# Kernel tuning notes

Hardware: AMD Instinct MI355X
Metric: run time of the kernel (lower is better)

Reference implementation:

```python
import jax, jax.numpy as jnp
import numpy as np

N, T, E, D, U = 32, 2048, 512, 1024, 256


def setup_inputs() -> dict:
    key = jax.random.key(0)
    ks = jax.random.split(key, 6)
    queries = jax.random.normal(ks[0], (N, 1, D), dtype=jnp.float32)
    prev = jax.random.uniform(ks[1], (N, T), dtype=jnp.float32)
    prev = prev / jnp.sum(prev, axis=1, keepdims=True)  # distribution-like initial alignment
    memory = jax.random.normal(ks[2], (N, T, E), dtype=jnp.float32)
    W_q = jax.random.normal(ks[3], (D, U), dtype=jnp.float32) * (1.0 / np.sqrt(D))
    W_k = jax.random.normal(ks[4], (E, U), dtype=jnp.float32) * (1.0 / np.sqrt(E))
    v = jax.random.uniform(ks[5], (U,), dtype=jnp.float32)
    return {"queries": queries, "previous_alignments": prev, "memory": memory,
            "W_q": W_q, "W_k": W_k, "v": v}


def safe_cumprod_exclusive(x):
    # exclusive cumprod via log-space cumsum, clamped like the torch original
    logsum = jnp.cumsum(jnp.log(jnp.clip(x, 1e-20, 1.0)), axis=1)  # [N,T]
    excl = jnp.concatenate([jnp.zeros_like(logsum[:, :1]), logsum], axis=1)[:, :-1]
    return jnp.exp(excl)


def reference(queries, previous_alignments, memory, W_q, W_k, v):
    # Bahdanau additive score (normalize=False path)
    proj_key = jnp.einsum('bte,eu->btu', memory, W_k)          # set_memory
    proj_q = jnp.einsum('bqd,du->bqu', queries, W_q)           # [N,1,U]
    weights = jnp.einsum('btu,u->bt', jnp.tanh(proj_q + proj_key), v)  # [N,T]
    p_choose = jax.nn.sigmoid(weights)
    # monotonic attention recursion in cumsum/cumprod form
    cumprod_1mp = safe_cumprod_exclusive(1.0 - p_choose)
    alignments = p_choose * cumprod_1mp * jnp.cumsum(
        previous_alignments / jnp.clip(cumprod_1mp, 1e-10, 1.0), axis=1)
    contexts = jnp.einsum('bt,bte->be', alignments, memory)    # bmm + squeeze
    return (contexts, alignments)
```

## Files before the change

kernel.cpp:

```cpp
#include <hip/hip_runtime.h>
#include <math.h>

#define N_ 32
#define T_ 2048
#define E_ 512
#define D_ 1024
#define U_ 256
#define PQ_CH 4

typedef __attribute__((ext_vector_type(8))) short bf16x8;
typedef __attribute__((ext_vector_type(16))) float f32x16;

__device__ __forceinline__ short f2bf_rne(float x) {
  unsigned int u = __float_as_uint(x);
  unsigned int r = u + 0x7FFFu + ((u >> 16) & 1u);
  return (short)(r >> 16);
}
__device__ __forceinline__ short f2bf_trunc(float x) {
  return (short)(__float_as_uint(x) >> 16);
}
__device__ __forceinline__ float bf2f(short h) {
  return __uint_as_float(((unsigned int)(unsigned short)h) << 16);
}

__global__ __launch_bounds__(256) void wk_pack_kernel(
    const float* __restrict__ Wk, bf16x8* __restrict__ whiP, bf16x8* __restrict__ wloP) {
  const int fid = blockIdx.x * 256 + threadIdx.x;
  const int lane = fid & 63;
  const int ub = (fid >> 6) & 7;
  const int kc = (fid >> 9) & 3;
  const int c = fid >> 11;
  const int u = ub * 32 + (lane & 31);
  const int e0 = c * 64 + kc * 16 + (lane >> 5) * 8;
  bf16x8 H, L;
#pragma unroll
  for (int j = 0; j < 8; ++j) {
    float x = Wk[(size_t)(e0 + j) * U_ + u];
    short h = f2bf_trunc(x);
    H[j] = h;
    L[j] = f2bf_rne(x - bf2f(h));
  }
  whiP[fid] = H;
  wloP[fid] = L;
}

__global__ __launch_bounds__(256) void projq_partial_kernel(
    const float* __restrict__ queries, const float* __restrict__ W_q,
    float* __restrict__ pq_part) {
  const int b = blockIdx.y, ch = blockIdx.x, tid = threadIdx.x;
  const int d0 = ch * (D_ / PQ_CH);
  const float* q = queries + b * D_ + d0;
  const float* wq = W_q + (size_t)d0 * U_ + tid;
  float acc = 0.f;
#pragma unroll 8
  for (int d = 0; d < D_ / PQ_CH; ++d)
    acc = fmaf(q[d], wq[(size_t)d * U_], acc);
  pq_part[((b * PQ_CH) + ch) * U_ + tid] = acc;
}

__global__ __launch_bounds__(256) void projq_reduce_kernel(
    const float* __restrict__ pq_part, float* __restrict__ proj_q) {
  const int b = blockIdx.x, tid = threadIdx.x;
  float s = 0.f;
#pragma unroll
  for (int c = 0; c < PQ_CH; ++c) s += pq_part[((b * PQ_CH) + c) * U_ + tid];
  proj_q[b * U_ + tid] = s;
}

__global__ __launch_bounds__(256, 2) void score_kernel(
    const float* __restrict__ memory, const bf16x8* __restrict__ whiP,
    const bf16x8* __restrict__ wloP, const float* __restrict__ proj_q,
    const float* __restrict__ v, float* __restrict__ p_choose) {
  __shared__ short sAhi[2][128 * 64];
  __shared__ short sAlo[2][128 * 64];
  __shared__ float smem_w[4][128];

  const int b = blockIdx.y;
  const int t0 = blockIdx.x * 128;
  const int tid = threadIdx.x;
  const int lane = tid & 63;
  const int ty = tid >> 6;
  const int l31 = lane & 31;
  const int half = lane >> 5;

  f32x16 acc[4][2];
#pragma unroll
  for (int mt = 0; mt < 4; ++mt)
#pragma unroll
    for (int nt = 0; nt < 2; ++nt)
#pragma unroll
      for (int r = 0; r < 16; ++r) acc[mt][nt][r] = 0.f;

  const int sr = tid >> 1;
  const int cs = (tid & 1) * 32;
  const float* srow = memory + ((size_t)(b * T_ + t0 + sr)) * E_ + cs;

  float4 xr[8];
  auto load_chunk = [&](int it) {
    const float* src = srow + it * 64;
#pragma unroll
    for (int j = 0; j < 8; ++j) xr[j] = *(const float4*)(src + j * 4);
  };
  auto stage_chunk = [&](int p) {
    char* bh = (char*)&sAhi[p][0] + sr * 128;
    char* bl = (char*)&sAlo[p][0] + sr * 128;
#pragma unroll
    for (int j = 0; j < 4; ++j) {
      float xs[8] = {xr[2 * j].x, xr[2 * j].y, xr[2 * j].z, xr[2 * j].w,
                     xr[2 * j + 1].x, xr[2 * j + 1].y, xr[2 * j + 1].z, xr[2 * j + 1].w};
      bf16x8 H, L;
#pragma unroll
      for (int i = 0; i < 8; ++i) {
        short h = f2bf_trunc(xs[i]);
        H[i] = h;
        L[i] = f2bf_rne(xs[i] - bf2f(h));
      }
      const int slot = (((tid & 1) * 4 + j) ^ (sr & 7)) * 16;
      *(bf16x8*)(bh + slot) = H;
      *(bf16x8*)(bl + slot) = L;
    }
  };

  load_chunk(0);
  stage_chunk(0);
  __syncthreads();

  for (int it = 0; it < 8; ++it) {
    const int p = it & 1;
    if (it < 7) load_chunk(it + 1);
#pragma unroll
    for (int kc = 0; kc < 4; ++kc) {
      bf16x8 bh[2], bl[2];
#pragma unroll
      for (int nt = 0; nt < 2; ++nt) {
        const int fidx = ((it * 4 + kc) * 8 + (ty * 2 + nt)) * 64 + lane;
        bh[nt] = whiP[fidx];
        bl[nt] = wloP[fidx];
      }
      bf16x8 ah[4], al[4];
#pragma unroll
      for (int mt = 0; mt < 4; ++mt) {
        const int m = mt * 32 + l31;
        const int off = m * 128 + (((kc * 2 + half) ^ (m & 7)) * 16);
        ah[mt] = *(const bf16x8*)((const char*)&sAhi[p][0] + off);
        al[mt] = *(const bf16x8*)((const char*)&sAlo[p][0] + off);
      }
#pragma unroll
      for (int mt = 0; mt < 4; ++mt)
#pragma unroll
        for (int nt = 0; nt < 2; ++nt) {
          acc[mt][nt] = __builtin_amdgcn_mfma_f32_32x32x16_bf16(ah[mt], bh[nt], acc[mt][nt], 0, 0, 0);
          acc[mt][nt] = __builtin_amdgcn_mfma_f32_32x32x16_bf16(ah[mt], bl[nt], acc[mt][nt], 0, 0, 0);
          acc[mt][nt] = __builtin_amdgcn_mfma_f32_32x32x16_bf16(al[mt], bh[nt], acc[mt][nt], 0, 0, 0);
        }
    }
    if (it < 7) {
      stage_chunk(p ^ 1);
      __syncthreads();
    }
  }

  const int u0 = ty * 64 + l31;
  const int u1 = ty * 64 + 32 + l31;
  const float pq0 = proj_q[b * U_ + u0], pq1 = proj_q[b * U_ + u1];
  const float v0 = v[u0], v1 = v[u1];

#pragma unroll
  for (int mt = 0; mt < 4; ++mt)
#pragma unroll
    for (int r = 0; r < 16; ++r) {
      float s = tanhf(acc[mt][0][r] + pq0) * v0 + tanhf(acc[mt][1][r] + pq1) * v1;
#pragma unroll
      for (int off = 1; off < 32; off <<= 1) s += __shfl_xor(s, off, 64);
      if (l31 == 0) {
        const int row = mt * 32 + (r & 3) + 8 * (r >> 2) + 4 * half;
        smem_w[ty][row] = s;
      }
    }
  __syncthreads();
  if (tid < 128) {
    const float w = smem_w[0][tid] + smem_w[1][tid] + smem_w[2][tid] + smem_w[3][tid];
    p_choose[b * T_ + t0 + tid] = 1.0f / (1.0f + expf(-w));
  }
}

__device__ __forceinline__ float block_incl_scan(float val, float* sbuf, int tid) {
  float x = val;
  sbuf[tid] = x;
  __syncthreads();
#pragma unroll
  for (int off = 1; off < 256; off <<= 1) {
    float t = (tid >= off) ? sbuf[tid - off] : 0.f;
    __syncthreads();
    x += t;
    sbuf[tid] = x;
    __syncthreads();
  }
  return x;
}

__global__ __launch_bounds__(256) void scan_kernel(
    const float* __restrict__ p_choose, const float* __restrict__ prev,
    float* __restrict__ align_out) {
  __shared__ float sbuf[256];
  const int b = blockIdx.x, tid = threadIdx.x;
  const int base = b * T_ + tid * 8;
  float4 p0 = *(const float4*)(p_choose + base);
  float4 p1 = *(const float4*)(p_choose + base + 4);
  float p[8] = {p0.x, p0.y, p0.z, p0.w, p1.x, p1.y, p1.z, p1.w};
  float s[8];
  float run = 0.f;
#pragma unroll
  for (int k = 0; k < 8; ++k) {
    float x = 1.0f - p[k];
    x = fminf(fmaxf(x, 1e-20f), 1.0f);
    run += logf(x);
    s[k] = run;
  }
  float incl = block_incl_scan(run, sbuf, tid);
  float excl = incl - run;
  float cp[8];
#pragma unroll
  for (int k = 0; k < 8; ++k)
    cp[k] = expf(excl + (k ? s[k - 1] : 0.f));
  float4 r0 = *(const float4*)(prev + base);
  float4 r1 = *(const float4*)(prev + base + 4);
  float pr[8] = {r0.x, r0.y, r0.z, r0.w, r1.x, r1.y, r1.z, r1.w};
  float s2[8];
  float run2 = 0.f;
#pragma unroll
  for (int k = 0; k < 8; ++k) {
    float d = fminf(fmaxf(cp[k], 1e-10f), 1.0f);
    run2 += pr[k] / d;
    s2[k] = run2;
  }
  float incl2 = block_incl_scan(run2, sbuf, tid);
  float excl2 = incl2 - run2;
#pragma unroll
  for (int k = 0; k < 8; ++k)
    p[k] = p[k] * cp[k] * (excl2 + s2[k]);
  *(float4*)(align_out + base) = make_float4(p[0], p[1], p[2], p[3]);
  *(float4*)(align_out + base + 4) = make_float4(p[4], p[5], p[6], p[7]);
}

__global__ __launch_bounds__(256) void ctx_partial_kernel(
    const float* __restrict__ memory, const float* __restrict__ align,
    float* __restrict__ partials) {
  const int b = blockIdx.y, ch = blockIdx.x, tid = threadIdx.x;
  const int tg = tid >> 7;
  const int col = (tid & 127) * 4;
  const int t0 = ch * 256 + tg * 128;
  const float* mrow = memory + ((size_t)(b * T_ + t0)) * E_ + col;
  const float* arow = align + b * T_ + t0;
  float4 a = make_float4(0.f, 0.f, 0.f, 0.f);
#pragma unroll 4
  for (int t = 0; t < 128; ++t) {
    float al = arow[t];
    float4 m = *(const float4*)(mrow + (size_t)t * E_);
    a.x = fmaf(al, m.x, a.x);
    a.y = fmaf(al, m.y, a.y);
    a.z = fmaf(al, m.z, a.z);
    a.w = fmaf(al, m.w, a.w);
  }
  *(float4*)(partials + ((size_t)(b * 16 + ch * 2 + tg)) * E_ + col) = a;
}

__global__ __launch_bounds__(256) void ctx_reduce_kernel(
    const float* __restrict__ partials, float* __restrict__ ctx) {
  const int b = blockIdx.x, tid = threadIdx.x;
#pragma unroll
  for (int e = tid; e < E_; e += 256) {
    float s = 0.f;
#pragma unroll
    for (int c = 0; c < 16; ++c) s += partials[((size_t)(b * 16 + c)) * E_ + e];
    ctx[b * E_ + e] = s;
  }
}

extern "C" void kernel_launch(void* const* d_in, const int* in_sizes, int n_in,
                              void* d_out, int out_size, void* d_ws, size_t ws_size,
                              hipStream_t stream) {
  (void)in_sizes; (void)n_in; (void)out_size; (void)ws_size;
  const float* queries = (const float*)d_in[0];
  const float* prev    = (const float*)d_in[1];
  const float* memory  = (const float*)d_in[2];
  const float* W_q     = (const float*)d_in[3];
  const float* W_k     = (const float*)d_in[4];
  const float* v       = (const float*)d_in[5];

  float* out = (float*)d_out;
  float* ctx_out = out;
  float* align_out = out + N_ * E_;

  float* ws = (float*)d_ws;
  bf16x8* whiP     = (bf16x8*)ws;
  bf16x8* wloP     = (bf16x8*)(ws + 65536);
  float* p_choose  = ws + 131072;
  float* proj_q    = ws + 196608;
  float* pq_part   = ws + 204800;
  float* ctx_parts = ws;

  wk_pack_kernel<<<dim3(64), 256, 0, stream>>>(W_k, whiP, wloP);
  projq_partial_kernel<<<dim3(PQ_CH, N_), 256, 0, stream>>>(queries, W_q, pq_part);
  projq_reduce_kernel<<<dim3(N_), 256, 0, stream>>>(pq_part, proj_q);
  score_kernel<<<dim3(T_ / 128, N_), 256, 0, stream>>>(memory, whiP, wloP, proj_q, v, p_choose);
  scan_kernel<<<dim3(N_), 256, 0, stream>>>(p_choose, prev, align_out);
  ctx_partial_kernel<<<dim3(8, N_), 256, 0, stream>>>(memory, align_out, ctx_parts);
  ctx_reduce_kernel<<<dim3(N_), 256, 0, stream>>>(ctx_parts, ctx_out);
}
```

Measured before the change: 286.3 us.

## Fuse prep kernels, drop score double-buffering, use atomics for context reduction

Merges the W_k packing and the query-projection partial kernels into one launch, and folds the proj_q reduction into the score kernel's epilogue. The score kernel moves from a double-buffered LDS pipeline to a single buffer with two barriers per chunk, which halves its LDS use but no longer overlaps global loads with MFMA work. The context reduction kernel is replaced by float atomicAdds from 512 blocks, with the scan kernel zeroing the output first. This removes three launches, but the atomic sums make results order-dependent and the loss of prefetch may slow the dominant score kernel.

```diff
diff --git a/kernel.cpp b/kernel.cpp
--- a/kernel.cpp
+++ b/kernel.cpp
@@ -6,7 +6,6 @@
 #define E_ 512
 #define D_ 1024
 #define U_ 256
-#define PQ_CH 4
 
 typedef __attribute__((ext_vector_type(8))) short bf16x8;
 typedef __attribute__((ext_vector_type(16))) float f32x16;
@@ -23,56 +22,52 @@
   return __uint_as_float(((unsigned int)(unsigned short)h) << 16);
 }
 
-__global__ __launch_bounds__(256) void wk_pack_kernel(
-    const float* __restrict__ Wk, bf16x8* __restrict__ whiP, bf16x8* __restrict__ wloP) {
-  const int fid = blockIdx.x * 256 + threadIdx.x;
-  const int lane = fid & 63;
-  const int ub = (fid >> 6) & 7;
-  const int kc = (fid >> 9) & 3;
-  const int c = fid >> 11;
-  const int u = ub * 32 + (lane & 31);
-  const int e0 = c * 64 + kc * 16 + (lane >> 5) * 8;
-  bf16x8 H, L;
-#pragma unroll
-  for (int j = 0; j < 8; ++j) {
-    float x = Wk[(size_t)(e0 + j) * U_ + u];
-    short h = f2bf_trunc(x);
-    H[j] = h;
-    L[j] = f2bf_rne(x - bf2f(h));
-  }
-  whiP[fid] = H;
-  wloP[fid] = L;
-}
-
-__global__ __launch_bounds__(256) void projq_partial_kernel(
-    const float* __restrict__ queries, const float* __restrict__ W_q,
-    float* __restrict__ pq_part) {
-  const int b = blockIdx.y, ch = blockIdx.x, tid = threadIdx.x;
-  const int d0 = ch * (D_ / PQ_CH);
-  const float* q = queries + b * D_ + d0;
-  const float* wq = W_q + (size_t)d0 * U_ + tid;
-  float acc = 0.f;
+__global__ __launch_bounds__(256) void prep_kernel(
+    const float* __restrict__ Wk, const float* __restrict__ queries,
+    const float* __restrict__ Wq, bf16x8* __restrict__ whiP,
+    bf16x8* __restrict__ wloP, float* __restrict__ pq_part) {
+  const int wg = blockIdx.x, tid = threadIdx.x;
+  if (wg < 64) {
+    const int fid = wg * 256 + tid;
+    const int lane = fid & 63;
+    const int ub = (fid >> 6) & 7;
+    const int kc = (fid >> 9) & 3;
+    const int c = fid >> 11;
+    const int u = ub * 32 + (lane & 31);
+    const int e0 = c * 64 + kc * 16 + (lane >> 5) * 8;
+    bf16x8 H, L;
+#pragma unroll
+    for (int j = 0; j < 8; ++j) {
+      float x = Wk[(size_t)(e0 + j) * U_ + u];
+      short h = f2bf_trunc(x);
+      H[j] = h;
+      L[j] = f2bf_rne(x - bf2f(h));
+    }
+    whiP[fid] = H;
+    wloP[fid] = L;
+  } else {
+    const int id = wg - 64;
+    const int ch = id & 3;
+    const int b = id >> 2;
+    const int bb = (wg - 64) >> 2;
+    const int d0 = ch * 256;
+    const float* q = queries + bb * D_ + d0;
+    const float* wq = Wq + (size_t)d0 * U_ + tid;
+    float acc = 0.f;
 #pragma unroll 8
-  for (int d = 0; d < D_ / PQ_CH; ++d)
-    acc = fmaf(q[d], wq[(size_t)d * U_], acc);
-  pq_part[((b * PQ_CH) + ch) * U_ + tid] = acc;
-}
-
-__global__ __launch_bounds__(256) void projq_reduce_kernel(
-    const float* __restrict__ pq_part, float* __restrict__ proj_q) {
-  const int b = blockIdx.x, tid = threadIdx.x;
-  float s = 0.f;
-#pragma unroll
-  for (int c = 0; c < PQ_CH; ++c) s += pq_part[((b * PQ_CH) + c) * U_ + tid];
-  proj_q[b * U_ + tid] = s;
+    for (int d = 0; d < 256; ++d)
+      acc = fmaf(q[d], wq[(size_t)d * U_], acc);
+    pq_part[(bb * 4 + ch) * U_ + tid] = acc;
+    (void)b;
+  }
 }
 
 __global__ __launch_bounds__(256, 2) void score_kernel(
     const float* __restrict__ memory, const bf16x8* __restrict__ whiP,
-    const bf16x8* __restrict__ wloP, const float* __restrict__ proj_q,
+    const bf16x8* __restrict__ wloP, const float* __restrict__ pq_part,
     const float* __restrict__ v, float* __restrict__ p_choose) {
-  __shared__ short sAhi[2][128 * 64];
-  __shared__ short sAlo[2][128 * 64];
+  __shared__ short sAhi[128 * 64];
+  __shared__ short sAlo[128 * 64];
   __shared__ float smem_w[4][128];
 
   const int b = blockIdx.y;
@@ -95,39 +90,33 @@
   const int cs = (tid & 1) * 32;
   const float* srow = memory + ((size_t)(b * T_ + t0 + sr)) * E_ + cs;
 
-  float4 xr[8];
-  auto load_chunk = [&](int it) {
+  for (int it = 0; it < 8; ++it) {
+    float4 xr[8];
     const float* src = srow + it * 64;
 #pragma unroll
     for (int j = 0; j < 8; ++j) xr[j] = *(const float4*)(src + j * 4);
-  };
-  auto stage_chunk = [&](int p) {
-    char* bh = (char*)&sAhi[p][0] + sr * 128;
-    char* bl = (char*)&sAlo[p][0] + sr * 128;
-#pragma unroll
-    for (int j = 0; j < 4; ++j) {
-      float xs[8] = {xr[2 * j].x, xr[2 * j].y, xr[2 * j].z, xr[2 * j].w,
-                     xr[2 * j + 1].x, xr[2 * j + 1].y, xr[2 * j + 1].z, xr[2 * j + 1].w};
-      bf16x8 H, L;
-#pragma unroll
-      for (int i = 0; i < 8; ++i) {
-        short h = f2bf_trunc(xs[i]);
-        H[i] = h;
-        L[i] = f2bf_rne(xs[i] - bf2f(h));
-      }
-      const int slot = (((tid & 1) * 4 + j) ^ (sr & 7)) * 16;
-      *(bf16x8*)(bh + slot) = H;
-      *(bf16x8*)(bl + slot) = L;
-    }
-  };
-
-  load_chunk(0);
-  stage_chunk(0);
-  __syncthreads();
-
-  for (int it = 0; it < 8; ++it) {
-    const int p = it & 1;
-    if (it < 7) load_chunk(it + 1);
+    __syncthreads();
+    {
+      char* bhp = (char*)sAhi + sr * 128;
+      char* blp = (char*)sAlo + sr * 128;
+#pragma unroll
+      for (int j = 0; j < 4; ++j) {
+        float xs[8] = {xr[2 * j].x, xr[2 * j].y, xr[2 * j].z, xr[2 * j].w,
+                       xr[2 * j + 1].x, xr[2 * j + 1].y, xr[2 * j + 1].z, xr[2 * j + 1].w};
+        bf16x8 H, L;
+#pragma unroll
+        for (int i = 0; i < 8; ++i) {
+          short h = f2bf_trunc(xs[i]);
+          H[i] = h;
+          L[i] = f2bf_rne(xs[i] - bf2f(h));
+        }
+        const int slot = (((tid & 1) * 4 + j) ^ (sr & 7)) * 16;
+        *(bf16x8*)(bhp + slot) = H;
+        *(bf16x8*)(blp + slot) = L;
+      }
+    }
+    __syncthreads();
+
 #pragma unroll
     for (int kc = 0; kc < 4; ++kc) {
       bf16x8 bh[2], bl[2];
@@ -142,8 +131,8 @@
       for (int mt = 0; mt < 4; ++mt) {
         const int m = mt * 32 + l31;
         const int off = m * 128 + (((kc * 2 + half) ^ (m & 7)) * 16);
-        ah[mt] = *(const bf16x8*)((const char*)&sAhi[p][0] + off);
-        al[mt] = *(const bf16x8*)((const char*)&sAlo[p][0] + off);
+        ah[mt] = *(const bf16x8*)((const char*)sAhi + off);
+        al[mt] = *(const bf16x8*)((const char*)sAlo + off);
       }
 #pragma unroll
       for (int mt = 0; mt < 4; ++mt)
@@ -154,17 +143,17 @@
           acc[mt][nt] = __builtin_amdgcn_mfma_f32_32x32x16_bf16(al[mt], bh[nt], acc[mt][nt], 0, 0, 0);
         }
     }
-    if (it < 7) {
-      stage_chunk(p ^ 1);
-      __syncthreads();
-    }
   }
 
   const int u0 = ty * 64 + l31;
-  const int u1 = ty * 64 + 32 + l31;
-  const float pq0 = proj_q[b * U_ + u0], pq1 = proj_q[b * U_ + u1];
+  const int u1 = u0 + 32;
+  float pq0 = 0.f, pq1 = 0.f;
+#pragma unroll
+  for (int c = 0; c < 4; ++c) {
+    pq0 += pq_part[(b * 4 + c) * U_ + u0];
+    pq1 += pq_part[(b * 4 + c) * U_ + u1];
+  }
   const float v0 = v[u0], v1 = v[u1];
-
 #pragma unroll
   for (int mt = 0; mt < 4; ++mt)
 #pragma unroll
@@ -201,9 +190,11 @@
 
 __global__ __launch_bounds__(256) void scan_kernel(
     const float* __restrict__ p_choose, const float* __restrict__ prev,
-    float* __restrict__ align_out) {
+    float* __restrict__ align_out, float* __restrict__ ctx_out) {
   __shared__ float sbuf[256];
   const int b = blockIdx.x, tid = threadIdx.x;
+  ctx_out[b * E_ + tid] = 0.f;
+  ctx_out[b * E_ + 256 + tid] = 0.f;
   const int base = b * T_ + tid * 8;
   float4 p0 = *(const float4*)(p_choose + base);
   float4 p1 = *(const float4*)(p_choose + base + 4);
@@ -243,18 +234,18 @@
   *(float4*)(align_out + base + 4) = make_float4(p[4], p[5], p[6], p[7]);
 }
 
-__global__ __launch_bounds__(256) void ctx_partial_kernel(
+__global__ __launch_bounds__(256) void ctx_kernel(
     const float* __restrict__ memory, const float* __restrict__ align,
-    float* __restrict__ partials) {
-  const int b = blockIdx.y, ch = blockIdx.x, tid = threadIdx.x;
-  const int tg = tid >> 7;
+    float* __restrict__ ctx_out) {
+  const int wg = blockIdx.x, tid = threadIdx.x;
+  const int b = wg >> 4;
+  const int t0 = (wg & 15) * 128 + (tid >> 7) * 64;
   const int col = (tid & 127) * 4;
-  const int t0 = ch * 256 + tg * 128;
   const float* mrow = memory + ((size_t)(b * T_ + t0)) * E_ + col;
   const float* arow = align + b * T_ + t0;
   float4 a = make_float4(0.f, 0.f, 0.f, 0.f);
 #pragma unroll 4
-  for (int t = 0; t < 128; ++t) {
+  for (int t = 0; t < 64; ++t) {
     float al = arow[t];
     float4 m = *(const float4*)(mrow + (size_t)t * E_);
     a.x = fmaf(al, m.x, a.x);
@@ -262,19 +253,11 @@
     a.z = fmaf(al, m.z, a.z);
     a.w = fmaf(al, m.w, a.w);
   }
-  *(float4*)(partials + ((size_t)(b * 16 + ch * 2 + tg)) * E_ + col) = a;
-}
-
-__global__ __launch_bounds__(256) void ctx_reduce_kernel(
-    const float* __restrict__ partials, float* __restrict__ ctx) {
-  const int b = blockIdx.x, tid = threadIdx.x;
-#pragma unroll
-  for (int e = tid; e < E_; e += 256) {
-    float s = 0.f;
-#pragma unroll
-    for (int c = 0; c < 16; ++c) s += partials[((size_t)(b * 16 + c)) * E_ + e];
-    ctx[b * E_ + e] = s;
-  }
+  float* dst = ctx_out + b * E_ + col;
+  atomicAdd(dst + 0, a.x);
+  atomicAdd(dst + 1, a.y);
+  atomicAdd(dst + 2, a.z);
+  atomicAdd(dst + 3, a.w);
 }
 
 extern "C" void kernel_launch(void* const* d_in, const int* in_sizes, int n_in,
@@ -284,8 +267,8 @@
   const float* queries = (const float*)d_in[0];
   const float* prev    = (const float*)d_in[1];
   const float* memory  = (const float*)d_in[2];
-  const float* W_q     = (const float*)d_in[3];
-  const float* W_k     = (const float*)d_in[4];
+  const float* Wq      = (const float*)d_in[3];
+  const float* Wk      = (const float*)d_in[4];
   const float* v       = (const float*)d_in[5];
 
   float* out = (float*)d_out;
@@ -293,18 +276,13 @@
   float* align_out = out + N_ * E_;
 
   float* ws = (float*)d_ws;
-  bf16x8* whiP     = (bf16x8*)ws;
-  bf16x8* wloP     = (bf16x8*)(ws + 65536);
-  float* p_choose  = ws + 131072;
-  float* proj_q    = ws + 196608;
-  float* pq_part   = ws + 204800;
-  float* ctx_parts = ws;
-
-  wk_pack_kernel<<<dim3(64), 256, 0, stream>>>(W_k, whiP, wloP);
-  projq_partial_kernel<<<dim3(PQ_CH, N_), 256, 0, stream>>>(queries, W_q, pq_part);
-  projq_reduce_kernel<<<dim3(N_), 256, 0, stream>>>(pq_part, proj_q);
-  score_kernel<<<dim3(T_ / 128, N_), 256, 0, stream>>>(memory, whiP, wloP, proj_q, v, p_choose);
-  scan_kernel<<<dim3(N_), 256, 0, stream>>>(p_choose, prev, align_out);
-  ctx_partial_kernel<<<dim3(8, N_), 256, 0, stream>>>(memory, align_out, ctx_parts);
-  ctx_reduce_kernel<<<dim3(N_), 256, 0, stream>>>(ctx_parts, ctx_out);
-}
+  bf16x8* whiP    = (bf16x8*)ws;
+  bf16x8* wloP    = (bf16x8*)(ws + 65536);
+  float* p_choose = ws + 131072;
+  float* pq_part  = ws + 196608;
+
+  prep_kernel<<<dim3(64 + 128), 256, 0, stream>>>(Wk, queries, Wq, whiP, wloP, pq_part);
+  score_kernel<<<dim3(T_ / 128, N_), 256, 0, stream>>>(memory, whiP, wloP, pq_part, v, p_choose);
+  scan_kernel<<<dim3(N_), 256, 0, stream>>>(p_choose, prev, align_out, ctx_out);
+  ctx_kernel<<<dim3(512), 256, 0, stream>>>(memory, align_out, ctx_out);
+}
```

Result: no change. 286.1 us (-0.1%).
